# Kernel optimization log

Hardware: AMD Instinct MI355X
Metric: run time of the kernel (lower is better)

Reference implementation:

```python
import jax, jax.numpy as jnp
import numpy as np

N_NODES = 50000
N_EDGES = 800000
IN_DIM = 128
HID_DIM = 128
OUT_DIM = 128
NEG_SLOPE = 0.2


def setup_inputs() -> dict:
    key = jax.random.key(0)
    ks = jax.random.split(key, 12)
    x = jax.random.normal(ks[0], (N_NODES, IN_DIM), dtype=jnp.float32)
    edge_index = jax.random.randint(ks[1], (2, N_EDGES), 0, N_NODES, dtype=jnp.int64)
    edge_weight = jax.random.uniform(ks[2], (N_EDGES,), dtype=jnp.float32)
    # Glorot-ish init for weights, zeros for bias (PyG GATConv defaults)
    s1 = 1.0 / np.sqrt(IN_DIM)
    s2 = 1.0 / np.sqrt(HID_DIM)
    W1 = jax.random.normal(ks[3], (IN_DIM, HID_DIM), dtype=jnp.float32) * s1
    a_src1 = jax.random.normal(ks[4], (HID_DIM,), dtype=jnp.float32) * s2
    a_dst1 = jax.random.normal(ks[5], (HID_DIM,), dtype=jnp.float32) * s2
    b1 = jnp.zeros((HID_DIM,), dtype=jnp.float32)
    W2 = jax.random.normal(ks[6], (HID_DIM, OUT_DIM), dtype=jnp.float32) * s2
    a_src2 = jax.random.normal(ks[7], (OUT_DIM,), dtype=jnp.float32) * (1.0 / np.sqrt(OUT_DIM))
    a_dst2 = jax.random.normal(ks[8], (OUT_DIM,), dtype=jnp.float32) * (1.0 / np.sqrt(OUT_DIM))
    b2 = jnp.zeros((OUT_DIM,), dtype=jnp.float32)
    return {"x": x, "edge_index": edge_index, "edge_weight": edge_weight,
            "W1": W1, "a_src1": a_src1, "a_dst1": a_dst1, "b1": b1,
            "W2": W2, "a_src2": a_src2, "a_dst2": a_dst2, "b2": b2}


def _gat_layer(x, src, dst, W, a_src, a_dst, b, n_nodes):
    # Linear transform: [N, F_out]
    h = x @ W
    # Per-node attention logits (heads=1): scalar per node
    al_src = h @ a_src  # [N]
    al_dst = h @ a_dst  # [N]
    # Edge-wise raw attention, LeakyReLU(negative_slope=0.2)
    e = al_src[src] + al_dst[dst]                     # [E]
    e = jnp.where(e >= 0, e, NEG_SLOPE * e)
    # Numerically stable segment softmax over incoming edges of dst
    m = jax.ops.segment_max(e, dst, num_segments=n_nodes)   # [N]
    ex = jnp.exp(e - m[dst])                                # [E]
    denom = jax.ops.segment_sum(ex, dst, num_segments=n_nodes)  # [N]
    alpha = ex / denom[dst]                                 # [E]
    # Attention-weighted scatter-add aggregation
    out = jax.ops.segment_sum(alpha[:, None] * h[src], dst, num_segments=n_nodes)
    return out + b


def reference(x, edge_index, edge_weight, W1, a_src1, a_dst1, b1, W2, a_src2, a_dst2, b2):
    n = x.shape[0]
    # PyG GATConv default add_self_loops=True; edge_weight (edge_attr) is
    # ignored because edge_dim=None in GATConv(in, out, heads=1).
    loop = jnp.arange(n, dtype=edge_index.dtype)
    src = jnp.concatenate([edge_index[0], loop])
    dst = jnp.concatenate([edge_index[1], loop])
    h = jax.nn.relu(_gat_layer(x, src, dst, W1, a_src1, a_dst1, b1, n))
    out = jax.nn.relu(_gat_layer(h, src, dst, W2, a_src2, a_dst2, b2, n))
    return out
```

## Files before the change

kernel.cpp:

```cpp
#include <hip/hip_runtime.h>
#include <hip/hip_bf16.h>
#include <hip/hip_fp16.h>
#include <type_traits>

#define DIM 128
#define NEG_SLOPE 0.2f
#define LDSP 136
#define CAP 64
#define NXCD 8

typedef _Float16 half8 __attribute__((ext_vector_type(8)));
typedef float floatx4 __attribute__((ext_vector_type(4)));

__global__ __launch_bounds__(256) void prep_kernel(const float* __restrict__ W1,
                                                   _Float16* __restrict__ WT1,
                                                   const float* __restrict__ W2,
                                                   _Float16* __restrict__ WT2,
                                                   int* __restrict__ cnt, int n) {
    int b = blockIdx.x;
    int tid = threadIdx.x;
    if (b < 64) {
        int i = b * 256 + tid;
        int k = i >> 7, c = i & 127;
        WT1[c * DIM + k] = (_Float16)W1[i];
    } else if (b < 128) {
        int i = (b - 64) * 256 + tid;
        int k = i >> 7, c = i & 127;
        WT2[c * DIM + k] = (_Float16)W2[i];
    } else {
        int i = (b - 128) * 256 + tid;
        if (i < n) cnt[i] = 0;
    }
}

__global__ __launch_bounds__(256) void count_scatter_kernel(const int* __restrict__ src,
                                                            const int* __restrict__ dst,
                                                            int* __restrict__ cnt,
                                                            int* __restrict__ csr,
                                                            int E, int nPer) {
    int range = blockIdx.x & (NXCD - 1);
    int base = (blockIdx.x >> 3) * 2048;
    int lo = range * nPer;
    int hi = lo + nPer;
#pragma unroll
    for (int k = 0; k < 8; ++k) {
        int i = base + k * 256 + threadIdx.x;
        if (i < E) {
            int d = dst[i];
            if (d >= lo && d < hi) {
                int r = atomicAdd(&cnt[d], 1);
                if (r < CAP) csr[(size_t)d * CAP + r] = src[i];
            }
        }
    }
}

template <typename TIN>
__global__ __launch_bounds__(256, 4) void gemm_mfma_kernel(const TIN* __restrict__ X,
                                                           const _Float16* __restrict__ WT,
                                                           __half* __restrict__ Hh,
                                                           const float* __restrict__ a_src,
                                                           const float* __restrict__ a_dst,
                                                           float* __restrict__ alsrc,
                                                           float* __restrict__ aldst, int n) {
    __shared__ _Float16 Ws[DIM * LDSP];
    int tid = threadIdx.x;
    int row0 = blockIdx.x * 64;

    for (int e = tid * 8; e < DIM * DIM; e += 256 * 8) {
        int r = e >> 7, c = e & 127;
        *(uint4*)&Ws[r * LDSP + c] = *(const uint4*)&WT[r * DIM + c];
    }

    int lane = tid & 63;
    int w = tid >> 6;
    int lo = lane & 15, hi = lane >> 4;

    int arow = row0 + w * 16 + lo;
    int ar = (arow < n) ? arow : (n - 1);
    half8 av[4];
#pragma unroll
    for (int t = 0; t < 4; ++t) {
        if constexpr (std::is_same<TIN, float>::value) {
            float4 v0 = *(const float4*)&X[(size_t)ar * DIM + t * 32 + hi * 8];
            float4 v1 = *(const float4*)&X[(size_t)ar * DIM + t * 32 + hi * 8 + 4];
            half8 h = {(_Float16)v0.x, (_Float16)v0.y, (_Float16)v0.z, (_Float16)v0.w,
                       (_Float16)v1.x, (_Float16)v1.y, (_Float16)v1.z, (_Float16)v1.w};
            av[t] = h;
        } else {
            av[t] = *(const half8*)&X[(size_t)ar * DIM + t * 32 + hi * 8];
        }
    }
    __syncthreads();

    floatx4 acc[8] = {};
#pragma unroll
    for (int t = 0; t < 4; ++t) {
#pragma unroll
        for (int f = 0; f < 8; ++f) {
            half8 bv = *(half8*)&Ws[(f * 16 + lo) * LDSP + t * 32 + hi * 8];
            acc[f] = __builtin_amdgcn_mfma_f32_16x16x32_f16(av[t], bv, acc[f], 0, 0, 0);
        }
    }

    float als[8], ald[8];
#pragma unroll
    for (int f = 0; f < 8; ++f) {
        als[f] = a_src[f * 16 + lo];
        ald[f] = a_dst[f * 16 + lo];
    }
#pragma unroll
    for (int r = 0; r < 4; ++r) {
        int grow = row0 + w * 16 + hi * 4 + r;
        float ps = 0.f, pd = 0.f;
#pragma unroll
        for (int f = 0; f < 8; ++f) {
            float v = acc[f][r];
            ps = fmaf(v, als[f], ps);
            pd = fmaf(v, ald[f], pd);
        }
#pragma unroll
        for (int o = 1; o <= 8; o <<= 1) {
            ps += __shfl_xor(ps, o);
            pd += __shfl_xor(pd, o);
        }
        if (grow < n) {
#pragma unroll
            for (int f = 0; f < 8; ++f)
                Hh[(size_t)grow * DIM + f * 16 + lo] = __float2half(acc[f][r]);
            if (lo == 0) { alsrc[grow] = ps; aldst[grow] = pd; }
        }
    }
}

template <bool OUT16>
__global__ __launch_bounds__(256) void agg_kernel(const __half* __restrict__ Hh,
                                                  const int* __restrict__ cnt,
                                                  const int* __restrict__ csr,
                                                  const float* __restrict__ alsrc,
                                                  const float* __restrict__ aldst,
                                                  const float* __restrict__ bias,
                                                  void* __restrict__ OUTp, int n) {
    int wid = (blockIdx.x * 256 + threadIdx.x) >> 6;
    int lane = threadIdx.x & 63;
    if (wid >= n) return;

    int deg = cnt[wid];
    deg = (deg < CAP) ? deg : CAP;
    float ald = aldst[wid];

    float e_self = alsrc[wid] + ald;
    e_self = (e_self >= 0.f) ? e_self : NEG_SLOPE * e_self;

    int sIdx = 0;
    float eL = -INFINITY;
    if (lane < deg) {
        sIdx = csr[(size_t)wid * CAP + lane];
        float e = alsrc[sIdx] + ald;
        eL = (e >= 0.f) ? e : NEG_SLOPE * e;
    }
    float m = fmaxf(e_self, eL);
#pragma unroll
    for (int o = 32; o > 0; o >>= 1) m = fmaxf(m, __shfl_xor(m, o));

    float wL = (lane < deg) ? __expf(eL - m) : 0.f;
    float dsum = wL;
#pragma unroll
    for (int o = 32; o > 0; o >>= 1) dsum += __shfl_xor(dsum, o);

    float wS = __expf(e_self - m);
    float denom = wS + dsum;

    int half = lane >> 5;
    int fl = (lane & 31) * 4;
    float a0 = 0.f, a1 = 0.f, a2 = 0.f, a3 = 0.f;
    int degP = (deg + 1) & ~1;

    int j = 0;
    for (; j + 16 <= degP; j += 16) {
        int s[8]; float w[8]; uint2 h[8];
#pragma unroll
        for (int q = 0; q < 8; ++q) {
            int idx = j + 2 * q + half;
            s[q] = __shfl(sIdx, idx);
            w[q] = __shfl(wL, idx);
        }
#pragma unroll
        for (int q = 0; q < 8; ++q)
            h[q] = *(const uint2*)&Hh[(size_t)s[q] * DIM + fl];
#pragma unroll
        for (int q = 0; q < 8; ++q) {
            float2 fa = __half22float2(*(__half2*)&h[q].x);
            float2 fb = __half22float2(*(__half2*)&h[q].y);
            a0 = fmaf(w[q], fa.x, a0);
            a1 = fmaf(w[q], fa.y, a1);
            a2 = fmaf(w[q], fb.x, a2);
            a3 = fmaf(w[q], fb.y, a3);
        }
    }
    for (; j + 8 <= degP; j += 8) {
        int s[4]; float w[4]; uint2 h[4];
#pragma unroll
        for (int q = 0; q < 4; ++q) {
            int idx = j + 2 * q + half;
            s[q] = __shfl(sIdx, idx);
            w[q] = __shfl(wL, idx);
        }
#pragma unroll
        for (int q = 0; q < 4; ++q)
            h[q] = *(const uint2*)&Hh[(size_t)s[q] * DIM + fl];
#pragma unroll
        for (int q = 0; q < 4; ++q) {
            float2 fa = __half22float2(*(__half2*)&h[q].x);
            float2 fb = __half22float2(*(__half2*)&h[q].y);
            a0 = fmaf(w[q], fa.x, a0);
            a1 = fmaf(w[q], fa.y, a1);
            a2 = fmaf(w[q], fb.x, a2);
            a3 = fmaf(w[q], fb.y, a3);
        }
    }
    for (; j < degP; j += 2) {
        int idx = j + half;
        int s = __shfl(sIdx, idx);
        float w = __shfl(wL, idx);
        uint2 hr = *(const uint2*)&Hh[(size_t)s * DIM + fl];
        float2 fa = __half22float2(*(__half2*)&hr.x);
        float2 fb = __half22float2(*(__half2*)&hr.y);
        a0 = fmaf(w, fa.x, a0);
        a1 = fmaf(w, fa.y, a1);
        a2 = fmaf(w, fb.x, a2);
        a3 = fmaf(w, fb.y, a3);
    }

    a0 += __shfl_xor(a0, 32);
    a1 += __shfl_xor(a1, 32);
    a2 += __shfl_xor(a2, 32);
    a3 += __shfl_xor(a3, 32);

    if (half == 0) {
        uint2 hs = *(const uint2*)&Hh[(size_t)wid * DIM + fl];
        float2 ha = __half22float2(*(__half2*)&hs.x);
        float2 hb = __half22float2(*(__half2*)&hs.y);
        a0 = fmaf(wS, ha.x, a0);
        a1 = fmaf(wS, ha.y, a1);
        a2 = fmaf(wS, hb.x, a2);
        a3 = fmaf(wS, hb.y, a3);

        float inv = 1.0f / denom;
        float4 bv = *(const float4*)&bias[fl];
        float o0 = fmaxf(fmaf(a0, inv, bv.x), 0.0f);
        float o1 = fmaxf(fmaf(a1, inv, bv.y), 0.0f);
        float o2 = fmaxf(fmaf(a2, inv, bv.z), 0.0f);
        float o3 = fmaxf(fmaf(a3, inv, bv.w), 0.0f);
        if constexpr (OUT16) {
            __half2 p0 = __floats2half2_rn(o0, o1);
            __half2 p1 = __floats2half2_rn(o2, o3);
            uint2 u;
            u.x = *(unsigned int*)&p0;
            u.y = *(unsigned int*)&p1;
            *(uint2*)&((__half*)OUTp)[(size_t)wid * DIM + fl] = u;
        } else {
            *(float4*)&((float*)OUTp)[(size_t)wid * DIM + fl] = make_float4(o0, o1, o2, o3);
        }
    }
}

extern "C" void kernel_launch(void* const* d_in, const int* in_sizes, int n_in,
                              void* d_out, int out_size, void* d_ws, size_t ws_size,
                              hipStream_t stream) {
    const float* x      = (const float*)d_in[0];
    const int*   eidx   = (const int*)d_in[1];
    const float* W1     = (const float*)d_in[3];
    const float* asrc1  = (const float*)d_in[4];
    const float* adst1  = (const float*)d_in[5];
    const float* b1     = (const float*)d_in[6];
    const float* W2     = (const float*)d_in[7];
    const float* asrc2  = (const float*)d_in[8];
    const float* adst2  = (const float*)d_in[9];
    const float* b2     = (const float*)d_in[10];
    float* out = (float*)d_out;

    int n = in_sizes[0] / DIM;
    int E = in_sizes[1] / 2;
    const int* esrc = eidx;
    const int* edst = eidx + E;

    __half* Hh     = (__half*)d_ws;
    __half* y1h    = Hh + (size_t)n * DIM;
    _Float16* wt1  = (_Float16*)(y1h + (size_t)n * DIM);
    _Float16* wt2  = wt1 + DIM * DIM;
    float* alsrc   = (float*)(wt2 + DIM * DIM);
    float* aldst   = alsrc + n;
    int*   cnt     = (int*)(aldst + n);
    int*   csr     = cnt + n;

    int nPer = (n + NXCD - 1) / NXCD;
    int nslice = (E + 2047) / 2048;
    int gemm_grid = (n + 63) / 64;
    int wave_grid = (n + 3) / 4;

    prep_kernel<<<128 + (n + 255) / 256, 256, 0, stream>>>(W1, wt1, W2, wt2, cnt, n);

    count_scatter_kernel<<<nslice * NXCD, 256, 0, stream>>>(esrc, edst, cnt, csr, E, nPer);

    gemm_mfma_kernel<float><<<gemm_grid, 256, 0, stream>>>(x, wt1, Hh, asrc1, adst1, alsrc, aldst, n);
    agg_kernel<true><<<wave_grid, 256, 0, stream>>>(Hh, cnt, csr, alsrc, aldst, b1, y1h, n);

    gemm_mfma_kernel<_Float16><<<gemm_grid, 256, 0, stream>>>((const _Float16*)y1h, wt2, Hh, asrc2, adst2, alsrc, aldst, n);
    agg_kernel<false><<<wave_grid, 256, 0, stream>>>(Hh, cnt, csr, alsrc, aldst, b2, out, n);
}
```

Baseline: 149.5 us.

## Split per-node edge counters into four bins to reduce atomic contention

Each destination node now gets four counters and a 4x24-slot adjacency buffer, and a thread picks its bin from its thread index, so atomics on the same node spread over separate addresses. The scatter loop is also restructured to issue all loads, then all atomics, then all stores, which gives more memory-level parallelism. The aggregation kernel reads four counts and turns a lane index into a bin and slot. This costs extra counter zeroing, a larger CSR footprint and more index arithmetic in the aggregation. A skewed node can now drop edges once one bin passes 24 even when its total degree is under 64.

```diff
diff --git a/kernel.cpp b/kernel.cpp
--- a/kernel.cpp
+++ b/kernel.cpp
@@ -6,7 +6,9 @@
 #define DIM 128
 #define NEG_SLOPE 0.2f
 #define LDSP 136
-#define CAP 64
+#define NBIN 4
+#define SLOT 24
+#define CAP  (NBIN * SLOT)
 #define NXCD 8
 
 typedef _Float16 half8 __attribute__((ext_vector_type(8)));
@@ -16,7 +18,7 @@
                                                    _Float16* __restrict__ WT1,
                                                    const float* __restrict__ W2,
                                                    _Float16* __restrict__ WT2,
-                                                   int* __restrict__ cnt, int n) {
+                                                   int* __restrict__ cnt, int n4) {
     int b = blockIdx.x;
     int tid = threadIdx.x;
     if (b < 64) {
@@ -29,7 +31,7 @@
         WT2[c * DIM + k] = (_Float16)W2[i];
     } else {
         int i = (b - 128) * 256 + tid;
-        if (i < n) cnt[i] = 0;
+        if (i < n4) cnt[i] = 0;
     }
 }
 
@@ -37,20 +39,30 @@
                                                             const int* __restrict__ dst,
                                                             int* __restrict__ cnt,
                                                             int* __restrict__ csr,
-                                                            int E, int nPer) {
+                                                            int E, int nPer, int n) {
     int range = blockIdx.x & (NXCD - 1);
     int base = (blockIdx.x >> 3) * 2048;
     int lo = range * nPer;
     int hi = lo + nPer;
+    int tid = threadIdx.x;
+    int p = tid & (NBIN - 1);
+
+    int dd[8];
 #pragma unroll
     for (int k = 0; k < 8; ++k) {
-        int i = base + k * 256 + threadIdx.x;
-        if (i < E) {
-            int d = dst[i];
-            if (d >= lo && d < hi) {
-                int r = atomicAdd(&cnt[d], 1);
-                if (r < CAP) csr[(size_t)d * CAP + r] = src[i];
-            }
+        int i = base + k * 256 + tid;
+        dd[k] = (i < E) ? dst[i] : -1;
+        if (dd[k] < lo || dd[k] >= hi) dd[k] = -1;
+    }
+    int rr[8];
+#pragma unroll
+    for (int k = 0; k < 8; ++k)
+        rr[k] = (dd[k] >= 0) ? atomicAdd(&cnt[(size_t)p * n + dd[k]], 1) : SLOT;
+#pragma unroll
+    for (int k = 0; k < 8; ++k) {
+        if (dd[k] >= 0 && rr[k] < SLOT) {
+            int i = base + k * 256 + tid;
+            csr[(size_t)dd[k] * CAP + p * SLOT + rr[k]] = src[i];
         }
     }
 }
@@ -145,17 +157,31 @@
     int lane = threadIdx.x & 63;
     if (wid >= n) return;
 
-    int deg = cnt[wid];
-    deg = (deg < CAP) ? deg : CAP;
+    int c0 = cnt[wid];
+    int c1 = cnt[(size_t)n + wid];
+    int c2 = cnt[(size_t)2 * n + wid];
+    int c3 = cnt[(size_t)3 * n + wid];
+    c0 = (c0 < SLOT) ? c0 : SLOT;
+    c1 = (c1 < SLOT) ? c1 : SLOT;
+    c2 = (c2 < SLOT) ? c2 : SLOT;
+    c3 = (c3 < SLOT) ? c3 : SLOT;
+    int s01 = c0 + c1, s012 = s01 + c2;
+    int deg = s012 + c3;
+    deg = (deg < 64) ? deg : 64;
+
     float ald = aldst[wid];
-
     float e_self = alsrc[wid] + ald;
     e_self = (e_self >= 0.f) ? e_self : NEG_SLOPE * e_self;
 
     int sIdx = 0;
     float eL = -INFINITY;
     if (lane < deg) {
-        sIdx = csr[(size_t)wid * CAP + lane];
+        int bin, slot;
+        if (lane < c0)        { bin = 0; slot = lane; }
+        else if (lane < s01)  { bin = 1; slot = lane - c0; }
+        else if (lane < s012) { bin = 2; slot = lane - s01; }
+        else                  { bin = 3; slot = lane - s012; }
+        sIdx = csr[(size_t)wid * CAP + bin * SLOT + slot];
         float e = alsrc[sIdx] + ald;
         eL = (e >= 0.f) ? e : NEG_SLOPE * e;
     }
@@ -292,16 +318,17 @@
     float* alsrc   = (float*)(wt2 + DIM * DIM);
     float* aldst   = alsrc + n;
     int*   cnt     = (int*)(aldst + n);
-    int*   csr     = cnt + n;
+    int*   csr     = cnt + (size_t)NBIN * n;
 
     int nPer = (n + NXCD - 1) / NXCD;
     int nslice = (E + 2047) / 2048;
     int gemm_grid = (n + 63) / 64;
     int wave_grid = (n + 3) / 4;
-
-    prep_kernel<<<128 + (n + 255) / 256, 256, 0, stream>>>(W1, wt1, W2, wt2, cnt, n);
-
-    count_scatter_kernel<<<nslice * NXCD, 256, 0, stream>>>(esrc, edst, cnt, csr, E, nPer);
+    int n4 = NBIN * n;
+
+    prep_kernel<<<128 + (n4 + 255) / 256, 256, 0, stream>>>(W1, wt1, W2, wt2, cnt, n4);
+
+    count_scatter_kernel<<<nslice * NXCD, 256, 0, stream>>>(esrc, edst, cnt, csr, E, nPer, n);
 
     gemm_mfma_kernel<float><<<gemm_grid, 256, 0, stream>>>(x, wt1, Hh, asrc1, adst1, alsrc, aldst, n);
     agg_kernel<true><<<wave_grid, 256, 0, stream>>>(Hh, cnt, csr, alsrc, aldst, b1, y1h, n);
```

New measurement: 152.5 us. 2.1% more time.

## Fuse all GAT stages into one cooperative persistent kernel with grid syncs

Applied to the files above, without the earlier changes.

Replaces the six separate kernel launches with a single cooperative persistent kernel that uses grid-wide syncs between phases. Odd blocks build the CSR adjacency while even blocks run the first-layer GEMM at the same time, overlapping the scatter with the matrix multiply. This removes launch gaps and inter-kernel drain, in exchange for grid.sync costs and a grid capped by occupancy. Fewer resident blocks may also hurt latency hiding in the gather-heavy aggregation phases.

```diff
diff --git a/kernel.cpp b/kernel.cpp
--- a/kernel.cpp
+++ b/kernel.cpp
@@ -1,7 +1,10 @@
 #include <hip/hip_runtime.h>
+#include <hip/hip_cooperative_groups.h>
 #include <hip/hip_bf16.h>
 #include <hip/hip_fp16.h>
 #include <type_traits>
+
+namespace cg = cooperative_groups;
 
 #define DIM 128
 #define NEG_SLOPE 0.2f
@@ -12,66 +15,36 @@
 typedef _Float16 half8 __attribute__((ext_vector_type(8)));
 typedef float floatx4 __attribute__((ext_vector_type(4)));
 
-__global__ __launch_bounds__(256) void prep_kernel(const float* __restrict__ W1,
-                                                   _Float16* __restrict__ WT1,
-                                                   const float* __restrict__ W2,
-                                                   _Float16* __restrict__ WT2,
-                                                   int* __restrict__ cnt, int n) {
-    int b = blockIdx.x;
-    int tid = threadIdx.x;
-    if (b < 64) {
-        int i = b * 256 + tid;
-        int k = i >> 7, c = i & 127;
-        WT1[c * DIM + k] = (_Float16)W1[i];
-    } else if (b < 128) {
-        int i = (b - 64) * 256 + tid;
-        int k = i >> 7, c = i & 127;
-        WT2[c * DIM + k] = (_Float16)W2[i];
-    } else {
-        int i = (b - 128) * 256 + tid;
-        if (i < n) cnt[i] = 0;
-    }
-}
-
-__global__ __launch_bounds__(256) void count_scatter_kernel(const int* __restrict__ src,
-                                                            const int* __restrict__ dst,
-                                                            int* __restrict__ cnt,
-                                                            int* __restrict__ csr,
-                                                            int E, int nPer) {
-    int range = blockIdx.x & (NXCD - 1);
-    int base = (blockIdx.x >> 3) * 2048;
-    int lo = range * nPer;
-    int hi = lo + nPer;
-#pragma unroll
-    for (int k = 0; k < 8; ++k) {
-        int i = base + k * 256 + threadIdx.x;
-        if (i < E) {
-            int d = dst[i];
-            if (d >= lo && d < hi) {
-                int r = atomicAdd(&cnt[d], 1);
-                if (r < CAP) csr[(size_t)d * CAP + r] = src[i];
-            }
-        }
-    }
-}
-
-template <typename TIN>
-__global__ __launch_bounds__(256, 4) void gemm_mfma_kernel(const TIN* __restrict__ X,
-                                                           const _Float16* __restrict__ WT,
-                                                           __half* __restrict__ Hh,
-                                                           const float* __restrict__ a_src,
-                                                           const float* __restrict__ a_dst,
-                                                           float* __restrict__ alsrc,
-                                                           float* __restrict__ aldst, int n) {
-    __shared__ _Float16 Ws[DIM * LDSP];
-    int tid = threadIdx.x;
-    int row0 = blockIdx.x * 64;
-
-    for (int e = tid * 8; e < DIM * DIM; e += 256 * 8) {
+struct MegaArgs {
+    const float* x;
+    const int* esrc;
+    const int* edst;
+    const float* W1; const float* asrc1; const float* adst1; const float* b1;
+    const float* W2; const float* asrc2; const float* adst2; const float* b2;
+    float* out;
+    __half* Hh; __half* y1h;
+    _Float16* wt1; _Float16* wt2;
+    float* alsrc; float* aldst;
+    int* cnt; int* csr;
+    int n, E, nPer, nslice, ntile;
+};
+
+__device__ __forceinline__ void stage_W(const _Float16* __restrict__ WT, _Float16* Ws) {
+    for (int e = threadIdx.x * 8; e < DIM * DIM; e += 256 * 8) {
         int r = e >> 7, c = e & 127;
         *(uint4*)&Ws[r * LDSP + c] = *(const uint4*)&WT[r * DIM + c];
     }
-
+}
+
+template <typename TIN>
+__device__ __forceinline__ void gemm_tile(int t, const TIN* __restrict__ X,
+                                          const _Float16* Ws, __half* __restrict__ Hh,
+                                          const float* __restrict__ a_src,
+                                          const float* __restrict__ a_dst,
+                                          float* __restrict__ alsrc,
+                                          float* __restrict__ aldst, int n) {
+    int tid = threadIdx.x;
+    int row0 = t * 64;
     int lane = tid & 63;
     int w = tid >> 6;
     int lo = lane & 15, hi = lane >> 4;
@@ -80,26 +53,25 @@
     int ar = (arow < n) ? arow : (n - 1);
     half8 av[4];
 #pragma unroll
-    for (int t = 0; t < 4; ++t) {
+    for (int tt = 0; tt < 4; ++tt) {
         if constexpr (std::is_same<TIN, float>::value) {
-            float4 v0 = *(const float4*)&X[(size_t)ar * DIM + t * 32 + hi * 8];
-            float4 v1 = *(const float4*)&X[(size_t)ar * DIM + t * 32 + hi * 8 + 4];
+            float4 v0 = *(const float4*)&X[(size_t)ar * DIM + tt * 32 + hi * 8];
+            float4 v1 = *(const float4*)&X[(size_t)ar * DIM + tt * 32 + hi * 8 + 4];
             half8 h = {(_Float16)v0.x, (_Float16)v0.y, (_Float16)v0.z, (_Float16)v0.w,
                        (_Float16)v1.x, (_Float16)v1.y, (_Float16)v1.z, (_Float16)v1.w};
-            av[t] = h;
+            av[tt] = h;
         } else {
-            av[t] = *(const half8*)&X[(size_t)ar * DIM + t * 32 + hi * 8];
-        }
-    }
-    __syncthreads();
+            av[tt] = *(const half8*)&X[(size_t)ar * DIM + tt * 32 + hi * 8];
+        }
+    }
 
     floatx4 acc[8] = {};
 #pragma unroll
-    for (int t = 0; t < 4; ++t) {
+    for (int tt = 0; tt < 4; ++tt) {
 #pragma unroll
         for (int f = 0; f < 8; ++f) {
-            half8 bv = *(half8*)&Ws[(f * 16 + lo) * LDSP + t * 32 + hi * 8];
-            acc[f] = __builtin_amdgcn_mfma_f32_16x16x32_f16(av[t], bv, acc[f], 0, 0, 0);
+            half8 bv = *(const half8*)&Ws[(f * 16 + lo) * LDSP + tt * 32 + hi * 8];
+            acc[f] = __builtin_amdgcn_mfma_f32_16x16x32_f16(av[tt], bv, acc[f], 0, 0, 0);
         }
     }
 
@@ -134,17 +106,14 @@
 }
 
 template <bool OUT16>
-__global__ __launch_bounds__(256) void agg_kernel(const __half* __restrict__ Hh,
-                                                  const int* __restrict__ cnt,
-                                                  const int* __restrict__ csr,
-                                                  const float* __restrict__ alsrc,
-                                                  const float* __restrict__ aldst,
-                                                  const float* __restrict__ bias,
-                                                  void* __restrict__ OUTp, int n) {
-    int wid = (blockIdx.x * 256 + threadIdx.x) >> 6;
-    int lane = threadIdx.x & 63;
-    if (wid >= n) return;
-
+__device__ __forceinline__ void agg_node(int wid, int lane,
+                                         const __half* __restrict__ Hh,
+                                         const int* __restrict__ cnt,
+                                         const int* __restrict__ csr,
+                                         const float* __restrict__ alsrc,
+                                         const float* __restrict__ aldst,
+                                         const float* __restrict__ bias,
+                                         void* __restrict__ OUTp, int n) {
     int deg = cnt[wid];
     deg = (deg < CAP) ? deg : CAP;
     float ald = aldst[wid];
@@ -265,6 +234,78 @@
     }
 }
 
+__global__ __launch_bounds__(256, 4) void mega_kernel(MegaArgs a) {
+    __shared__ _Float16 Ws[DIM * LDSP];
+    cg::grid_group grid = cg::this_grid();
+    int nb = gridDim.x;
+    int b = blockIdx.x;
+    int tid = threadIdx.x;
+    int gthread = b * 256 + tid;
+    int nthreads = nb * 256;
+
+    for (int i = gthread; i < a.n; i += nthreads) a.cnt[i] = 0;
+    for (int i = gthread; i < DIM * DIM; i += nthreads) {
+        int k = i >> 7, c = i & 127;
+        a.wt1[c * DIM + k] = (_Float16)a.W1[i];
+        a.wt2[c * DIM + k] = (_Float16)a.W2[i];
+    }
+    grid.sync();
+
+    if (b & 1) {
+        int c = (b >> 1) & (NXCD - 1);
+        int lo = c * a.nPer, hi = lo + a.nPer;
+        for (int s = (b >> 4); s < a.nslice; s += (nb >> 4)) {
+            int base = s * 2048;
+#pragma unroll
+            for (int k = 0; k < 8; ++k) {
+                int i = base + k * 256 + tid;
+                if (i < a.E) {
+                    int d = a.edst[i];
+                    if (d >= lo && d < hi) {
+                        int r = atomicAdd(&a.cnt[d], 1);
+                        if (r < CAP) a.csr[(size_t)d * CAP + r] = a.esrc[i];
+                    }
+                }
+            }
+        }
+    } else {
+        int t0 = b >> 1, ts = nb >> 1;
+        if (t0 < a.ntile) {
+            stage_W(a.wt1, Ws);
+            __syncthreads();
+            for (int t = t0; t < a.ntile; t += ts)
+                gemm_tile<float>(t, a.x, Ws, a.Hh, a.asrc1, a.adst1, a.alsrc, a.aldst, a.n);
+        }
+    }
+    grid.sync();
+
+    {
+        int lane = tid & 63;
+        int wid0 = b * 4 + (tid >> 6);
+        for (int wid = wid0; wid < a.n; wid += nb * 4)
+            agg_node<true>(wid, lane, a.Hh, a.cnt, a.csr, a.alsrc, a.aldst, a.b1, a.y1h, a.n);
+    }
+    grid.sync();
+
+    {
+        if (b < a.ntile) {
+            stage_W(a.wt2, Ws);
+            __syncthreads();
+            for (int t = b; t < a.ntile; t += nb)
+                gemm_tile<_Float16>(t, (const _Float16*)a.y1h, Ws, a.Hh,
+                                    a.asrc2, a.adst2, a.alsrc, a.aldst, a.n);
+        }
+    }
+    grid.sync();
+
+    {
+        int lane = tid & 63;
+        int wid0 = b * 4 + (tid >> 6);
+        for (int wid = wid0; wid < a.n; wid += nb * 4)
+            agg_node<false>(wid, lane, a.Hh, a.cnt, a.csr, a.alsrc, a.aldst, a.b2, a.out, a.n);
+    }
+}
+
 extern "C" void kernel_launch(void* const* d_in, const int* in_sizes, int n_in,
                               void* d_out, int out_size, void* d_ws, size_t ws_size,
                               hipStream_t stream) {
@@ -282,8 +323,6 @@
 
     int n = in_sizes[0] / DIM;
     int E = in_sizes[1] / 2;
-    const int* esrc = eidx;
-    const int* edst = eidx + E;
 
     __half* Hh     = (__half*)d_ws;
     __half* y1h    = Hh + (size_t)n * DIM;
@@ -294,18 +333,26 @@
     int*   cnt     = (int*)(aldst + n);
     int*   csr     = cnt + n;
 
-    int nPer = (n + NXCD - 1) / NXCD;
-    int nslice = (E + 2047) / 2048;
-    int gemm_grid = (n + 63) / 64;
-    int wave_grid = (n + 3) / 4;
-
-    prep_kernel<<<128 + (n + 255) / 256, 256, 0, stream>>>(W1, wt1, W2, wt2, cnt, n);
-
-    count_scatter_kernel<<<nslice * NXCD, 256, 0, stream>>>(esrc, edst, cnt, csr, E, nPer);
-
-    gemm_mfma_kernel<float><<<gemm_grid, 256, 0, stream>>>(x, wt1, Hh, asrc1, adst1, alsrc, aldst, n);
-    agg_kernel<true><<<wave_grid, 256, 0, stream>>>(Hh, cnt, csr, alsrc, aldst, b1, y1h, n);
-
-    gemm_mfma_kernel<_Float16><<<gemm_grid, 256, 0, stream>>>((const _Float16*)y1h, wt2, Hh, asrc2, adst2, alsrc, aldst, n);
-    agg_kernel<false><<<wave_grid, 256, 0, stream>>>(Hh, cnt, csr, alsrc, aldst, b2, out, n);
-}
+    MegaArgs ma;
+    ma.x = x; ma.esrc = eidx; ma.edst = eidx + E;
+    ma.W1 = W1; ma.asrc1 = asrc1; ma.adst1 = adst1; ma.b1 = b1;
+    ma.W2 = W2; ma.asrc2 = asrc2; ma.adst2 = adst2; ma.b2 = b2;
+    ma.out = out; ma.Hh = Hh; ma.y1h = y1h;
+    ma.wt1 = wt1; ma.wt2 = wt2;
+    ma.alsrc = alsrc; ma.aldst = aldst;
+    ma.cnt = cnt; ma.csr = csr;
+    ma.n = n; ma.E = E;
+    ma.nPer = (n + NXCD - 1) / NXCD;
+    ma.nslice = (E + 2047) / 2048;
+    ma.ntile = (n + 63) / 64;
+
+    int maxB = 0;
+    hipError_t oe = hipOccupancyMaxActiveBlocksPerMultiprocessor(&maxB, mega_kernel, 256, 0);
+    int nb = (oe == hipSuccess && maxB > 0) ? maxB * 256 : 512;
+    if (nb > 2048) nb = 2048;
+    nb &= ~15;
+    if (nb < 16) nb = 16;
+
+    void* args[] = { &ma };
+    hipLaunchCooperativeKernel((void*)mega_kernel, dim3(nb), dim3(256), args, 0, stream);
+}
```

Result: slower. 496.0 us (+231.9%).

## Replace global-atomic CSR build with two-pass bucketed LDS-atomic construction

Applied to the files above, without the earlier changes.

Edges are first partitioned into 256 destination-range buckets using per-block LDS histograms and one global atomic per bucket per block. A second kernel then builds each bucket's per-node adjacency lists with LDS atomics. This is meant to replace per-edge global atomics on node counters and the 8x redundant edge scan. In exchange it adds an intermediate arena write and read, a fixed per-bucket capacity that silently drops edges beyond it, and a build pass limited to 256 blocks.

```diff
diff --git a/kernel.cpp b/kernel.cpp
--- a/kernel.cpp
+++ b/kernel.cpp
@@ -7,7 +7,8 @@
 #define NEG_SLOPE 0.2f
 #define LDSP 136
 #define CAP 64
-#define NXCD 8
+#define NB 256
+#define ABUCKET 4096
 
 typedef _Float16 half8 __attribute__((ext_vector_type(8)));
 typedef float floatx4 __attribute__((ext_vector_type(4)));
@@ -16,7 +17,7 @@
                                                    _Float16* __restrict__ WT1,
                                                    const float* __restrict__ W2,
                                                    _Float16* __restrict__ WT2,
-                                                   int* __restrict__ cnt, int n) {
+                                                   int* __restrict__ gcur) {
     int b = blockIdx.x;
     int tid = threadIdx.x;
     if (b < 64) {
@@ -28,29 +29,83 @@
         int k = i >> 7, c = i & 127;
         WT2[c * DIM + k] = (_Float16)W2[i];
     } else {
-        int i = (b - 128) * 256 + tid;
-        if (i < n) cnt[i] = 0;
-    }
-}
-
-__global__ __launch_bounds__(256) void count_scatter_kernel(const int* __restrict__ src,
-                                                            const int* __restrict__ dst,
-                                                            int* __restrict__ cnt,
-                                                            int* __restrict__ csr,
-                                                            int E, int nPer) {
-    int range = blockIdx.x & (NXCD - 1);
-    int base = (blockIdx.x >> 3) * 2048;
-    int lo = range * nPer;
-    int hi = lo + nPer;
+        if (tid < NB) gcur[tid] = 0;
+    }
+}
+
+__global__ __launch_bounds__(256) void bucket_kernel(const int* __restrict__ src,
+                                                     const int* __restrict__ dst,
+                                                     int* __restrict__ gcur,
+                                                     int2* __restrict__ arena,
+                                                     int E, int npb) {
+    __shared__ int lhist[NB];
+    __shared__ int lbase[NB];
+    int tid = threadIdx.x;
+    if (tid < NB) lhist[tid] = 0;
+    __syncthreads();
+
+    int base = blockIdx.x * 2048;
+    int dd[8], ss[8], rk[8], bk[8];
 #pragma unroll
     for (int k = 0; k < 8; ++k) {
-        int i = base + k * 256 + threadIdx.x;
+        int i = base + k * 256 + tid;
         if (i < E) {
-            int d = dst[i];
-            if (d >= lo && d < hi) {
-                int r = atomicAdd(&cnt[d], 1);
-                if (r < CAP) csr[(size_t)d * CAP + r] = src[i];
-            }
+            dd[k] = dst[i];
+            ss[k] = src[i];
+            bk[k] = dd[k] / npb;
+            rk[k] = atomicAdd(&lhist[bk[k]], 1);
+        } else {
+            bk[k] = -1;
+        }
+    }
+    __syncthreads();
+
+    if (tid < NB) {
+        int c = lhist[tid];
+        lbase[tid] = c ? atomicAdd(&gcur[tid], c) : 0;
+    }
+    __syncthreads();
+
+#pragma unroll
+    for (int k = 0; k < 8; ++k) {
+        if (bk[k] >= 0) {
+            int pos = lbase[bk[k]] + rk[k];
+            if (pos < ABUCKET)
+                arena[(size_t)bk[k] * ABUCKET + pos] = make_int2(dd[k], ss[k]);
+        }
+    }
+}
+
+__global__ __launch_bounds__(1024) void build_kernel(const int2* __restrict__ arena,
+                                                     const int* __restrict__ gcur,
+                                                     int* __restrict__ cnt,
+                                                     int* __restrict__ csr,
+                                                     int n, int npb) {
+    __shared__ int lcnt[NB];
+    int B = blockIdx.x;
+    int tid = threadIdx.x;
+    int dlo = B * npb;
+
+    if (tid < npb) lcnt[tid] = 0;
+    __syncthreads();
+
+    int cntE = gcur[B];
+    if (cntE > ABUCKET) cntE = ABUCKET;
+    for (int i = tid; i < cntE; i += 1024) {
+        int2 e = arena[(size_t)B * ABUCKET + i];
+        int li = e.x - dlo;
+        if (li >= 0 && li < npb) {
+            int r = atomicAdd(&lcnt[li], 1);
+            if (r < CAP) csr[(size_t)e.x * CAP + r] = e.y;
+        }
+    }
+    __syncthreads();
+
+    if (tid < npb) {
+        int d = dlo + tid;
+        if (d < n) {
+            int c = lcnt[tid];
+            cnt[d] = (c < CAP) ? c : CAP;
         }
     }
 }
@@ -285,6 +340,8 @@
     const int* esrc = eidx;
     const int* edst = eidx + E;
 
+    int npb = (n + NB - 1) / NB;
+
     __half* Hh     = (__half*)d_ws;
     __half* y1h    = Hh + (size_t)n * DIM;
     _Float16* wt1  = (_Float16*)(y1h + (size_t)n * DIM);
@@ -293,15 +350,17 @@
     float* aldst   = alsrc + n;
     int*   cnt     = (int*)(aldst + n);
     int*   csr     = cnt + n;
-
-    int nPer = (n + NXCD - 1) / NXCD;
-    int nslice = (E + 2047) / 2048;
+    int*   gcur    = csr + (size_t)n * CAP;
+    int2*  arena   = (int2*)(gcur + NB);
+
     int gemm_grid = (n + 63) / 64;
     int wave_grid = (n + 3) / 4;
-
-    prep_kernel<<<128 + (n + 255) / 256, 256, 0, stream>>>(W1, wt1, W2, wt2, cnt, n);
-
-    count_scatter_kernel<<<nslice * NXCD, 256, 0, stream>>>(esrc, edst, cnt, csr, E, nPer);
+    int nbucket_blocks = (E + 2047) / 2048;
+
+    prep_kernel<<<129, 256, 0, stream>>>(W1, wt1, W2, wt2, gcur);
+
+    bucket_kernel<<<nbucket_blocks, 256, 0, stream>>>(esrc, edst, gcur, arena, E, npb);
+    build_kernel<<<NB, 1024, 0, stream>>>(arena, gcur, cnt, csr, n, npb);
 
     gemm_mfma_kernel<float><<<gemm_grid, 256, 0, stream>>>(x, wt1, Hh, asrc1, adst1, alsrc, aldst, n);
     agg_kernel<true><<<wave_grid, 256, 0, stream>>>(Hh, cnt, csr, alsrc, aldst, b1, y1h, n);
```

Measured after the change: 132.6 us. 1.13x faster.
